# Optimization experiments

Hardware: AMD Instinct MI355X
Metric: run time of the kernel (lower is better)

## Reference

```python
import jax, jax.numpy as jnp
import numpy as np

N = 131072      # total nodes per branch
G = 4096        # graphs in batch
NPG = 32        # nodes per graph
E = 1048576     # edges per branch (avg degree 8)
S = 64          # state_size
H = 128         # hidden_size
OUT = 1         # out_size
NEG_SLOPE = 0.2


def _make_edges(key):
    k1, k2, k3 = jax.random.split(key, 3)
    base = jax.random.randint(k1, (E,), 0, G) * NPG
    src = base + jax.random.randint(k2, (E,), 0, NPG)
    dst = base + jax.random.randint(k3, (E,), 0, NPG)
    return jnp.stack([src, dst]).astype(jnp.int64)


def setup_inputs() -> dict:
    key = jax.random.key(0)
    ks = jax.random.split(key, 12)
    batch = (jnp.arange(N) // NPG).astype(jnp.int64)
    return {
        "up_x": jax.random.normal(ks[0], (N, S), jnp.float32),
        "up_edge_index": _make_edges(ks[1]),
        "up_batch": batch,
        "down_x": jax.random.normal(ks[2], (N, S), jnp.float32),
        "down_edge_index": _make_edges(ks[3]),
        "down_batch": batch,
        "up_W": jax.random.normal(ks[4], (S, H), jnp.float32) / np.sqrt(S),
        "up_att_src": jax.random.normal(ks[5], (H,), jnp.float32) / np.sqrt(H),
        "up_att_dst": jax.random.normal(ks[6], (H,), jnp.float32) / np.sqrt(H),
        "up_bias": jnp.zeros((H,), jnp.float32),
        "down_W": jax.random.normal(ks[7], (S, H), jnp.float32) / np.sqrt(S),
        "down_att_src": jax.random.normal(ks[8], (H,), jnp.float32) / np.sqrt(H),
        "down_att_dst": jax.random.normal(ks[9], (H,), jnp.float32) / np.sqrt(H),
        "down_bias": jnp.zeros((H,), jnp.float32),
        "mlp_W": jax.random.normal(ks[10], (H, OUT), jnp.float32) / np.sqrt(H),
        "mlp_b": jnp.zeros((OUT,), jnp.float32),
    }


def _gat_conv(x, edge_index, W, att_src, att_dst, bias):
    # PyG GATConv, heads=1, add_self_loops=False
    h = x @ W                                  # [N, H]
    src, dst = edge_index[0], edge_index[1]
    a_src = h @ att_src                        # [N]
    a_dst = h @ att_dst                        # [N]
    e = jax.nn.leaky_relu(a_src[src] + a_dst[dst], NEG_SLOPE)  # [E]
    # segment softmax over incoming edges of each dst node
    m = jax.ops.segment_max(e, dst, num_segments=N)
    p = jnp.exp(e - m[dst])
    denom = jax.ops.segment_sum(p, dst, num_segments=N)
    alpha = p / (denom[dst] + 1e-16)
    out = jax.ops.segment_sum(alpha[:, None] * h[src], dst, num_segments=N)
    return out + bias


def _branch(x, edge_index, batch, W, att_src, att_dst, bias):
    h = _gat_conv(x, edge_index, W, att_src, att_dst, bias)
    num_nodes = jax.ops.segment_sum(jnp.ones_like(batch), batch, num_segments=G)
    self_idx = jnp.cumsum(num_nodes) - 1       # last node of each graph
    return jax.nn.sigmoid(h[self_idx])         # [G, H]


def reference(up_x, up_edge_index, up_batch, down_x, down_edge_index, down_batch,
              up_W, up_att_src, up_att_dst, up_bias,
              down_W, down_att_src, down_att_dst, down_bias,
              mlp_W, mlp_b):
    up = _branch(up_x, up_edge_index, up_batch, up_W, up_att_src, up_att_dst, up_bias)
    down = _branch(down_x, down_edge_index, down_batch, down_W, down_att_src, down_att_dst, down_bias)
    x = up * down
    return x @ mlp_W + mlp_b                   # [G, OUT]
```

## Files before the change

### kernel.cpp

```cpp
#include <hip/hip_runtime.h>
#include <math.h>

#define G_GRAPHS 4096
#define NPG 32
#define E_EDGES 1048576
#define S_DIM 64
#define H_DIM 128
#define CAP 128
#define NEG_SLOPE 0.2f


__global__ void init_kernel(int* __restrict__ cnt, float* __restrict__ wvec,
                            const float* __restrict__ upW, const float* __restrict__ upAs,
                            const float* __restrict__ upAd,
                            const float* __restrict__ dnW, const float* __restrict__ dnAs,
                            const float* __restrict__ dnAd) {
    int t = threadIdx.x;
    for (int i = t; i < 2 * G_GRAPHS; i += 256) cnt[i] = 0;
    int vec = t >> 6;
    int s   = t & 63;
    const float* W   = (vec < 2) ? upW : dnW;
    const float* att = (vec == 0) ? upAs : (vec == 1) ? upAd : (vec == 2) ? dnAs : dnAd;
    float acc = 0.f;
    for (int h = 0; h < H_DIM; ++h) acc += W[s * H_DIM + h] * att[h];
    wvec[vec * 64 + s] = acc;
}

__global__ void scan_kernel(const int* __restrict__ up_ei, const int* __restrict__ dn_ei,
                            int* __restrict__ cnt, int* __restrict__ buckets) {
    unsigned tid = blockIdx.x * blockDim.x + threadIdx.x;
    int branch = (tid >= E_EDGES) ? 1 : 0;
    unsigned e = branch ? (tid - E_EDGES) : tid;
    const int* ei = branch ? dn_ei : up_ei;
    int dst = ei[E_EDGES + e];
    if ((dst & (NPG - 1)) == NPG - 1) {
        int g = dst >> 5;
        int pos = atomicAdd(cnt + branch * G_GRAPHS + g, 1);
        if (pos < CAP) {
            int src = ei[e];
            buckets[(branch * G_GRAPHS + g) * CAP + pos] = src;
        }
    }
}

__global__ __launch_bounds__(128) void gat_kernel(
        const float* __restrict__ up_x, const float* __restrict__ dn_x,
        const float* __restrict__ upW, const float* __restrict__ dnW,
        const float* __restrict__ up_bias, const float* __restrict__ dn_bias,
        const float* __restrict__ mlp_W, const float* __restrict__ mlp_b,
        const int* __restrict__ cnt, const int* __restrict__ buckets,
        const float* __restrict__ wvec, float* __restrict__ out) {
    int g    = blockIdx.x;
    int wave = threadIdx.x >> 6;
    int lane = threadIdx.x & 63;

    __shared__ float evals[2][CAP];
    __shared__ float xsum_s[2][S_DIM];
    __shared__ float bout[2][H_DIM];

    const float* x    = wave ? dn_x : up_x;
    const float* W    = wave ? dnW : upW;
    const float* bias = wave ? dn_bias : up_bias;
    const float* wsrc = wvec + wave * 128;
    const float* wdst = wsrc + 64;

    int d = g * NPG + (NPG - 1);

    float v = x[d * S_DIM + lane] * wdst[lane];
    #pragma unroll
    for (int m = 32; m; m >>= 1) v += __shfl_xor(v, m, 64);
    float a_dst = v;

    int k = cnt[wave * G_GRAPHS + g];
    if (k > CAP) k = CAP;
    const int* bk = buckets + (wave * G_GRAPHS + g) * CAP;

    float mmax = -INFINITY;
    for (int i = 0; i < k; ++i) {
        int src = bk[i];
        float t = x[src * S_DIM + lane] * wsrc[lane];
        #pragma unroll
        for (int m = 32; m; m >>= 1) t += __shfl_xor(t, m, 64);
        float e = t + a_dst;
        e = (e > 0.f) ? e : NEG_SLOPE * e;
        if (lane == 0) evals[wave][i] = e;
        if (e > mmax) mmax = e;
    }

    float denom = 0.f, xs = 0.f;
    for (int i = 0; i < k; ++i) {
        float p = __expf(evals[wave][i] - mmax);
        int src = bk[i];
        xs += p * x[src * S_DIM + lane];
        denom += p;
    }
    xs /= (denom + 1e-16f);
    xsum_s[wave][lane] = xs;

    float o0 = bias[lane], o1 = bias[lane + 64];
    for (int s = 0; s < S_DIM; ++s) {
        float xv = xsum_s[wave][s];
        o0 += xv * W[s * H_DIM + lane];
        o1 += xv * W[s * H_DIM + lane + 64];
    }
    o0 = 1.f / (1.f + __expf(-o0));
    o1 = 1.f / (1.f + __expf(-o1));
    bout[wave][lane]      = o0;
    bout[wave][lane + 64] = o1;
    __syncthreads();

    if (wave == 0) {
        float part = bout[0][lane] * bout[1][lane] * mlp_W[lane]
                   + bout[0][lane + 64] * bout[1][lane + 64] * mlp_W[lane + 64];
        #pragma unroll
        for (int m = 32; m; m >>= 1) part += __shfl_xor(part, m, 64);
        if (lane == 0) out[g] = part + mlp_b[0];
    }
}

extern "C" void kernel_launch(void* const* d_in, const int* in_sizes, int n_in,
                              void* d_out, int out_size, void* d_ws, size_t ws_size,
                              hipStream_t stream) {
    const float* up_x  = (const float*)d_in[0];
    const int*   up_ei = (const int*)d_in[1];
    const float* dn_x  = (const float*)d_in[3];
    const int*   dn_ei = (const int*)d_in[4];
    const float* upW   = (const float*)d_in[6];
    const float* upAs  = (const float*)d_in[7];
    const float* upAd  = (const float*)d_in[8];
    const float* upB   = (const float*)d_in[9];
    const float* dnW   = (const float*)d_in[10];
    const float* dnAs  = (const float*)d_in[11];
    const float* dnAd  = (const float*)d_in[12];
    const float* dnB   = (const float*)d_in[13];
    const float* mlpW  = (const float*)d_in[14];
    const float* mlpB  = (const float*)d_in[15];
    float* out = (float*)d_out;

    int*   cnt     = (int*)d_ws;
    int*   buckets = cnt + 2 * G_GRAPHS;
    float* wvec    = (float*)(buckets + 2 * G_GRAPHS * CAP);

    init_kernel<<<1, 256, 0, stream>>>(cnt, wvec, upW, upAs, upAd, dnW, dnAs, dnAd);
    scan_kernel<<<(2 * E_EDGES) / 256, 256, 0, stream>>>(up_ei, dn_ei, cnt, buckets);
    gat_kernel<<<G_GRAPHS, 128, 0, stream>>>(up_x, dn_x, upW, dnW, upB, dnB,
                                             mlpW, mlpB, cnt, buckets, wvec, out);
}
```

Before: 164.8 us.

## Vectorize edge scan and restructure GAT gather to cache rows in registers

The scan kernel now reads destination indices as int4, so each thread handles four edges, and the branch index comes from a 2D grid. The GAT kernel processes four source rows per wave, each over 16 lanes using float4 loads, and keeps up to 32 rows in registers so the second pass does not gather them again. Softmax max and sum become parallel reductions. The init and output stages are also vectorized. This aims to cut serial per-edge latency and duplicate gathers, at the cost of more registers and more complex code.

```diff
diff --git a/kernel.cpp b/kernel.cpp
--- a/kernel.cpp
+++ b/kernel.cpp
@@ -7,38 +7,51 @@
 #define S_DIM 64
 #define H_DIM 128
 #define CAP 128
+#define MAXIT 8
 #define NEG_SLOPE 0.2f
 
 
-__global__ void init_kernel(int* __restrict__ cnt, float* __restrict__ wvec,
-                            const float* __restrict__ upW, const float* __restrict__ upAs,
-                            const float* __restrict__ upAd,
-                            const float* __restrict__ dnW, const float* __restrict__ dnAs,
-                            const float* __restrict__ dnAd) {
+__global__ __launch_bounds__(256) void init_kernel(
+        int* __restrict__ cnt, float* __restrict__ wvec,
+        const float* __restrict__ upW, const float* __restrict__ upAs,
+        const float* __restrict__ upAd,
+        const float* __restrict__ dnW, const float* __restrict__ dnAs,
+        const float* __restrict__ dnAd) {
     int t = threadIdx.x;
     for (int i = t; i < 2 * G_GRAPHS; i += 256) cnt[i] = 0;
     int vec = t >> 6;
     int s   = t & 63;
     const float* W   = (vec < 2) ? upW : dnW;
     const float* att = (vec == 0) ? upAs : (vec == 1) ? upAd : (vec == 2) ? dnAs : dnAd;
-    float acc = 0.f;
-    for (int h = 0; h < H_DIM; ++h) acc += W[s * H_DIM + h] * att[h];
-    wvec[vec * 64 + s] = acc;
-}
-
-__global__ void scan_kernel(const int* __restrict__ up_ei, const int* __restrict__ dn_ei,
-                            int* __restrict__ cnt, int* __restrict__ buckets) {
-    unsigned tid = blockIdx.x * blockDim.x + threadIdx.x;
-    int branch = (tid >= E_EDGES) ? 1 : 0;
-    unsigned e = branch ? (tid - E_EDGES) : tid;
+    const float4* Wr = (const float4*)(W + s * H_DIM);
+    const float4* A4 = (const float4*)att;
+    float a0 = 0.f, a1 = 0.f, a2 = 0.f, a3 = 0.f;
+    #pragma unroll
+    for (int h = 0; h < H_DIM / 4; ++h) {
+        float4 w = Wr[h], a = A4[h];
+        a0 += w.x * a.x; a1 += w.y * a.y; a2 += w.z * a.z; a3 += w.w * a.w;
+    }
+    wvec[vec * 64 + s] = (a0 + a1) + (a2 + a3);
+}
+
+__global__ __launch_bounds__(256) void scan_kernel(
+        const int* __restrict__ up_ei, const int* __restrict__ dn_ei,
+        int* __restrict__ cnt, int* __restrict__ buckets) {
+    int branch = blockIdx.y;
     const int* ei = branch ? dn_ei : up_ei;
-    int dst = ei[E_EDGES + e];
-    if ((dst & (NPG - 1)) == NPG - 1) {
-        int g = dst >> 5;
-        int pos = atomicAdd(cnt + branch * G_GRAPHS + g, 1);
-        if (pos < CAP) {
-            int src = ei[e];
-            buckets[(branch * G_GRAPHS + g) * CAP + pos] = src;
+    unsigned e4 = blockIdx.x * 256u + threadIdx.x;
+    int4 d4 = ((const int4*)(ei + E_EDGES))[e4];
+    int* bcnt  = cnt + branch * G_GRAPHS;
+    int* bbase = buckets + branch * G_GRAPHS * CAP;
+    unsigned e0 = e4 * 4u;
+    int ds[4] = {d4.x, d4.y, d4.z, d4.w};
+    #pragma unroll
+    for (int j = 0; j < 4; ++j) {
+        int dst = ds[j];
+        if ((dst & (NPG - 1)) == NPG - 1) {
+            int g = dst >> 5;
+            int pos = atomicAdd(bcnt + g, 1);
+            if (pos < CAP) bbase[g * CAP + pos] = ei[e0 + j];
         }
     }
 }
@@ -53,65 +66,126 @@
     int g    = blockIdx.x;
     int wave = threadIdx.x >> 6;
     int lane = threadIdx.x & 63;
+    int q    = lane >> 4;
+    int t    = lane & 15;
 
     __shared__ float evals[2][CAP];
     __shared__ float xsum_s[2][S_DIM];
     __shared__ float bout[2][H_DIM];
 
-    const float* x    = wave ? dn_x : up_x;
-    const float* W    = wave ? dnW : upW;
-    const float* bias = wave ? dn_bias : up_bias;
-    const float* wsrc = wvec + wave * 128;
-    const float* wdst = wsrc + 64;
+    const float*  x    = wave ? dn_x : up_x;
+    const float4* x4   = (const float4*)x;
+    const float*  W    = wave ? dnW : upW;
+    const float*  bias = wave ? dn_bias : up_bias;
+    const float*  wsrc = wvec + wave * 128;
+    const float4  ws4  = ((const float4*)wsrc)[t];
+    const float4  wd4  = ((const float4*)(wsrc + 64))[t];
 
     int d = g * NPG + (NPG - 1);
 
-    float v = x[d * S_DIM + lane] * wdst[lane];
-    #pragma unroll
-    for (int m = 32; m; m >>= 1) v += __shfl_xor(v, m, 64);
-    float a_dst = v;
+    float4 xd = x4[d * 16 + t];
+    float ad = xd.x * wd4.x + xd.y * wd4.y + xd.z * wd4.z + xd.w * wd4.w;
+    #pragma unroll
+    for (int m = 1; m < 16; m <<= 1) ad += __shfl_xor(ad, m, 64);
 
     int k = cnt[wave * G_GRAPHS + g];
     if (k > CAP) k = CAP;
     const int* bk = buckets + (wave * G_GRAPHS + g) * CAP;
+    int kk = (k + 3) >> 2;
+
+    float4 rows[MAXIT];
+    #pragma unroll
+    for (int it = 0; it < MAXIT; ++it) {
+        if (it >= kk) break;
+        int i = it * 4 + q;
+        bool valid = (i < k);
+        int src = bk[valid ? i : 0];
+        float4 xr = x4[src * 16 + t];
+        rows[it] = xr;
+        float e = xr.x * ws4.x + xr.y * ws4.y + xr.z * ws4.z + xr.w * ws4.w;
+        #pragma unroll
+        for (int m = 1; m < 16; m <<= 1) e += __shfl_xor(e, m, 64);
+        e += ad;
+        e = (e > 0.f) ? e : NEG_SLOPE * e;
+        if (valid && t == 0) evals[wave][i] = e;
+    }
+    for (int it = MAXIT; it < kk; ++it) {
+        int i = it * 4 + q;
+        bool valid = (i < k);
+        int src = bk[valid ? i : 0];
+        float4 xr = x4[src * 16 + t];
+        float e = xr.x * ws4.x + xr.y * ws4.y + xr.z * ws4.z + xr.w * ws4.w;
+        #pragma unroll
+        for (int m = 1; m < 16; m <<= 1) e += __shfl_xor(e, m, 64);
+        e += ad;
+        e = (e > 0.f) ? e : NEG_SLOPE * e;
+        if (valid && t == 0) evals[wave][i] = e;
+    }
 
     float mmax = -INFINITY;
-    for (int i = 0; i < k; ++i) {
-        int src = bk[i];
-        float t = x[src * S_DIM + lane] * wsrc[lane];
-        #pragma unroll
-        for (int m = 32; m; m >>= 1) t += __shfl_xor(t, m, 64);
-        float e = t + a_dst;
-        e = (e > 0.f) ? e : NEG_SLOPE * e;
-        if (lane == 0) evals[wave][i] = e;
-        if (e > mmax) mmax = e;
-    }
-
-    float denom = 0.f, xs = 0.f;
-    for (int i = 0; i < k; ++i) {
+    for (int i = lane; i < k; i += 64) mmax = fmaxf(mmax, evals[wave][i]);
+    #pragma unroll
+    for (int m = 32; m; m >>= 1) mmax = fmaxf(mmax, __shfl_xor(mmax, m, 64));
+    float denom = 0.f;
+    for (int i = lane; i < k; i += 64) {
         float p = __expf(evals[wave][i] - mmax);
-        int src = bk[i];
-        xs += p * x[src * S_DIM + lane];
+        evals[wave][i] = p;
         denom += p;
     }
-    xs /= (denom + 1e-16f);
-    xsum_s[wave][lane] = xs;
-
-    float o0 = bias[lane], o1 = bias[lane + 64];
+    #pragma unroll
+    for (int m = 32; m; m >>= 1) denom += __shfl_xor(denom, m, 64);
+    float inv = 1.f / (denom + 1e-16f);
+
+    float4 acc = {0.f, 0.f, 0.f, 0.f};
+    #pragma unroll
+    for (int it = 0; it < MAXIT; ++it) {
+        if (it >= kk) break;
+        int i = it * 4 + q;
+        float p = (i < k) ? evals[wave][i] : 0.f;
+        float4 xr = rows[it];
+        acc.x += p * xr.x; acc.y += p * xr.y; acc.z += p * xr.z; acc.w += p * xr.w;
+    }
+    for (int it = MAXIT; it < kk; ++it) {
+        int i = it * 4 + q;
+        bool valid = (i < k);
+        float p = valid ? evals[wave][i] : 0.f;
+        int src = bk[valid ? i : 0];
+        float4 xr = x4[src * 16 + t];
+        acc.x += p * xr.x; acc.y += p * xr.y; acc.z += p * xr.z; acc.w += p * xr.w;
+    }
+    #pragma unroll
+    for (int m = 16; m < 64; m <<= 1) {
+        acc.x += __shfl_xor(acc.x, m, 64);
+        acc.y += __shfl_xor(acc.y, m, 64);
+        acc.z += __shfl_xor(acc.z, m, 64);
+        acc.w += __shfl_xor(acc.w, m, 64);
+    }
+    if (lane < 16) {
+        float4 xs = {acc.x * inv, acc.y * inv, acc.z * inv, acc.w * inv};
+        ((float4*)xsum_s[wave])[lane] = xs;
+    }
+
+    const float2* W2 = (const float2*)W;
+    float2 bb = ((const float2*)bias)[lane];
+    float o0 = bb.x, o1 = bb.y;
+    #pragma unroll 8
     for (int s = 0; s < S_DIM; ++s) {
         float xv = xsum_s[wave][s];
-        o0 += xv * W[s * H_DIM + lane];
-        o1 += xv * W[s * H_DIM + lane + 64];
+        float2 w = W2[s * 64 + lane];
+        o0 += xv * w.x;
+        o1 += xv * w.y;
     }
     o0 = 1.f / (1.f + __expf(-o0));
     o1 = 1.f / (1.f + __expf(-o1));
-    bout[wave][lane]      = o0;
-    bout[wave][lane + 64] = o1;
+    bout[wave][2 * lane]     = o0;
+    bout[wave][2 * lane + 1] = o1;
     __syncthreads();
 
     if (wave == 0) {
-        float part = bout[0][lane] * bout[1][lane] * mlp_W[lane]
-                   + bout[0][lane + 64] * bout[1][lane + 64] * mlp_W[lane + 64];
+        float2 u  = ((const float2*)bout[0])[lane];
+        float2 dn = ((const float2*)bout[1])[lane];
+        float2 mw = ((const float2*)mlp_W)[lane];
+        float part = u.x * dn.x * mw.x + u.y * dn.y * mw.y;
         #pragma unroll
         for (int m = 32; m; m >>= 1) part += __shfl_xor(part, m, 64);
         if (lane == 0) out[g] = part + mlp_b[0];
@@ -142,7 +216,7 @@
     float* wvec    = (float*)(buckets + 2 * G_GRAPHS * CAP);
 
     init_kernel<<<1, 256, 0, stream>>>(cnt, wvec, upW, upAs, upAd, dnW, dnAs, dnAd);
-    scan_kernel<<<(2 * E_EDGES) / 256, 256, 0, stream>>>(up_ei, dn_ei, cnt, buckets);
+    scan_kernel<<<dim3(E_EDGES / 4 / 256, 2), 256, 0, stream>>>(up_ei, dn_ei, cnt, buckets);
     gat_kernel<<<G_GRAPHS, 128, 0, stream>>>(up_x, dn_x, upW, dnW, upB, dnB,
                                              mlpW, mlpB, cnt, buckets, wvec, out);
 }
```

Result: faster. 155.4 us (-5.7%).
